# Kernel tuning notes

Measured on AMD Instinct MI355X. Metric: run time of the kernel, lower is better.

The kernel has to match this reference:

```python
import jax, jax.numpy as jnp
import numpy as np

D_MODEL = 256
N_HEADS = 8
D_K = D_MODEL // N_HEADS


def setup_inputs() -> dict:
    key = jax.random.key(0)
    ks = jax.random.split(key, 9)
    s = 1.0 / np.sqrt(D_MODEL)
    x = jax.random.normal(ks[0], (2, 4096, D_MODEL), dtype=jnp.float32)
    Wq = jax.random.uniform(ks[1], (D_MODEL, D_MODEL), minval=-s, maxval=s)
    bq = jax.random.uniform(ks[2], (D_MODEL,), minval=-s, maxval=s)
    Wk = jax.random.uniform(ks[3], (D_MODEL, D_MODEL), minval=-s, maxval=s)
    bk = jax.random.uniform(ks[4], (D_MODEL,), minval=-s, maxval=s)
    Wv = jax.random.uniform(ks[5], (D_MODEL, D_MODEL), minval=-s, maxval=s)
    bv = jax.random.uniform(ks[6], (D_MODEL,), minval=-s, maxval=s)
    Wo = jax.random.uniform(ks[7], (D_MODEL, D_MODEL), minval=-s, maxval=s)
    bo = jax.random.uniform(ks[8], (D_MODEL,), minval=-s, maxval=s)
    return {"q": x, "Wq": Wq, "bq": bq, "Wk": Wk, "bk": bk,
            "Wv": Wv, "bv": bv, "Wo": Wo, "bo": bo}


def reference(q, Wq, bq, Wk, bk, Wv, bv, Wo, bo):
    B, L, _ = q.shape
    # nn.Linear: y = x @ W.T + b ; weights stored as [out, in]
    Q = (jnp.einsum('bld,ed->ble', q, Wq) + bq).reshape(B, L, N_HEADS, D_K).transpose(0, 2, 1, 3)
    K = (jnp.einsum('bld,ed->ble', q, Wk) + bk).reshape(B, L, N_HEADS, D_K).transpose(0, 2, 1, 3)
    V = (jnp.einsum('bld,ed->ble', q, Wv) + bv).reshape(B, L, N_HEADS, D_K).transpose(0, 2, 1, 3)
    scores = jnp.einsum('bhqd,bhkd->bhqk', Q, K) / jnp.sqrt(jnp.float32(D_K))
    attn = jax.nn.softmax(scores, axis=-1)  # dropout p=0 (eval): identity
    out = jnp.einsum('bhqk,bhkd->bhqd', attn, V)
    out = out.transpose(0, 2, 1, 3).reshape(B, L, D_MODEL)
    return jnp.einsum('bld,ed->ble', out, Wo) + bo
```

## Files before the change

kernel.cpp:

```cpp
#include <hip/hip_runtime.h>

#define D_MODEL 256
#define NH 8
#define DK 32
#define SEQ 4096
#define BATCH 2
#define M_ROWS (BATCH * SEQ)
#define QSCALE 0.17677669529663687f

typedef __attribute__((ext_vector_type(8))) short bf16x8;
typedef __attribute__((ext_vector_type(4))) short s16x4;
typedef __attribute__((ext_vector_type(4))) float f32x4;
typedef __attribute__((ext_vector_type(16))) float f32x16;

static __device__ __forceinline__ short f2bf(float f) {
    unsigned u = __float_as_uint(f);
    u += 0x7fff + ((u >> 16) & 1);
    return (short)(u >> 16);
}

__global__ void cvt_kernel(const float* __restrict__ src, short* __restrict__ dst, int n4) {
    int i = blockIdx.x * blockDim.x + threadIdx.x;
    if (i >= n4) return;
    float4 v = reinterpret_cast<const float4*>(src)[i];
    s16x4 o;
    o.x = f2bf(v.x); o.y = f2bf(v.y); o.z = f2bf(v.z); o.w = f2bf(v.w);
    reinterpret_cast<s16x4*>(dst)[i] = o;
}

__global__ void cvtw_kernel(const float* __restrict__ W0, const float* __restrict__ W1,
                            const float* __restrict__ W2, const float* __restrict__ W3,
                            short* __restrict__ D0, short* __restrict__ D1,
                            short* __restrict__ D2, short* __restrict__ D3) {
    const int seg = blockIdx.x >> 6;
    const int i = (blockIdx.x & 63) * blockDim.x + threadIdx.x;
    const float* s = seg == 0 ? W0 : seg == 1 ? W1 : seg == 2 ? W2 : W3;
    short* d = seg == 0 ? D0 : seg == 1 ? D1 : seg == 2 ? D2 : D3;
    float4 v = reinterpret_cast<const float4*>(s)[i];
    s16x4 o;
    o.x = f2bf(v.x); o.y = f2bf(v.y); o.z = f2bf(v.z); o.w = f2bf(v.w);
    reinterpret_cast<s16x4*>(d)[i] = o;
}

__global__ __launch_bounds__(256) void qkv_gemm(
    const short* __restrict__ A,
    const short* __restrict__ Wqb, const short* __restrict__ Wkb, const short* __restrict__ Wvb,
    const float* __restrict__ bq, const float* __restrict__ bk, const float* __restrict__ bv,
    short* __restrict__ Qb, short* __restrict__ Kblk, short* __restrict__ Vblk)
{
    const int ct = blockIdx.x;
    const int rt = blockIdx.y;
    const int tid = threadIdx.x;
    const int w = tid >> 6, l = tid & 63, l15 = l & 15, g = l >> 4;
    const int mat = ct >> 2;
    const int colbase = (ct & 3) * 64;
    const short* W = mat == 0 ? Wqb : mat == 1 ? Wkb : Wvb;
    const float* bias = mat == 0 ? bq : mat == 1 ? bk : bv;

    const int arow = rt * 64 + w * 16 + l15;
    f32x4 acc[4] = {};
#pragma unroll
    for (int ks = 0; ks < 8; ++ks) {
        bf16x8 af = *reinterpret_cast<const bf16x8*>(&A[(size_t)arow * 256 + ks * 32 + 8 * g]);
#pragma unroll
        for (int c = 0; c < 4; ++c) {
            const int col = colbase + 16 * c + l15;
            bf16x8 wf = *reinterpret_cast<const bf16x8*>(&W[(size_t)col * 256 + ks * 32 + 8 * g]);
            acc[c] = __builtin_amdgcn_mfma_f32_16x16x32_bf16(af, wf, acc[c], 0, 0, 0);
        }
    }

#pragma unroll
    for (int c = 0; c < 4; ++c) {
        const int col = colbase + 16 * c + l15;
        const float bv_ = bias[col];
#pragma unroll
        for (int r = 0; r < 4; ++r) {
            const int m = rt * 64 + w * 16 + 4 * g + r;
            const float v = acc[c][r] + bv_;
            const int head = col >> 5, d = col & 31;
            const int bb = m >> 12, seq = m & 4095;
            const size_t bhbase = (size_t)(bb * NH + head) * (SEQ * DK);
            if (mat == 0) {
                Qb[bhbase + (size_t)seq * 32 + d] = f2bf(v * QSCALE);
            } else if (mat == 1) {
                const int t = seq >> 6, s = (seq >> 5) & 1, lk = seq & 31;
                const int hh = (d >> 4) & 1, gk = (d >> 3) & 1, jk = d & 7;
                Kblk[bhbase + t * 2048 + (s * 2 + hh) * 512 + (gk * 32 + lk) * 8 + jk] = f2bf(v);
            } else {
                const int t = seq >> 6, w6 = seq & 63;
                const int c2 = w6 >> 4, gv = (w6 >> 2) & 1, jv = ((w6 >> 3) & 1) * 4 + (w6 & 3);
                Vblk[bhbase + t * 2048 + c2 * 512 + (gv * 32 + d) * 8 + jv] = f2bf(v);
            }
        }
    }
}

__global__ __launch_bounds__(128, 4) void attn_kernel(
    const short* __restrict__ Qb, const short* __restrict__ Kblk,
    const short* __restrict__ Vblk, short* __restrict__ AOb)
{
    __shared__ float accL[64][17];

    const int bid = ((int)blockIdx.x & 7) * 256 + ((int)blockIdx.x >> 3);
    const int qt = bid & 127;
    const int bh = bid >> 7;
    const int b = bh >> 3, h = bh & 7;
    const int w = threadIdx.x >> 6;
    const int l = threadIdx.x & 63;
    const int l31 = l & 31, g1 = l >> 5;

    const short* Qh = Qb + (size_t)bh * (SEQ * DK);
    const int q0 = qt * 32;
    const bf16x8 qf0 = *(const bf16x8*)&Qh[(size_t)(q0 + l31) * 32 + g1 * 8];
    const bf16x8 qf1 = *(const bf16x8*)&Qh[(size_t)(q0 + l31) * 32 + 16 + g1 * 8];

    const char* Kt = (const char*)Kblk + (size_t)bh * 262144 + (size_t)w * 131072 + l * 16;
    const char* Vt = (const char*)Vblk + (size_t)bh * 262144 + (size_t)w * 131072 + l * 16;

    f32x16 acc;
#pragma unroll
    for (int r = 0; r < 16; ++r) acc[r] = 0.f;
    float ls0 = 0.f, ls1 = 0.f, ls2 = 0.f, ls3 = 0.f;

    auto loadt = [&](bf16x8& K0, bf16x8& K1, bf16x8& K2, bf16x8& K3,
                     bf16x8& V0, bf16x8& V1, bf16x8& V2, bf16x8& V3, int tl) {
        const char* kp = Kt + (size_t)tl * 4096;
        const char* vp = Vt + (size_t)tl * 4096;
        K0 = *(const bf16x8*)(kp);        K1 = *(const bf16x8*)(kp + 1024);
        K2 = *(const bf16x8*)(kp + 2048); K3 = *(const bf16x8*)(kp + 3072);
        V0 = *(const bf16x8*)(vp);        V1 = *(const bf16x8*)(vp + 1024);
        V2 = *(const bf16x8*)(vp + 2048); V3 = *(const bf16x8*)(vp + 3072);
    };

    auto compute = [&](const bf16x8& K0, const bf16x8& K1, const bf16x8& K2, const bf16x8& K3,
                       const bf16x8& V0, const bf16x8& V1, const bf16x8& V2, const bf16x8& V3) {
        unsigned pk[2][8];
#pragma unroll
        for (int s = 0; s < 2; ++s) {
            f32x16 z;
#pragma unroll
            for (int r = 0; r < 16; ++r) z[r] = 0.f;
            z = __builtin_amdgcn_mfma_f32_32x32x16_bf16(s ? K2 : K0, qf0, z, 0, 0, 0);
            z = __builtin_amdgcn_mfma_f32_32x32x16_bf16(s ? K3 : K1, qf1, z, 0, 0, 0);
            float e[16];
#pragma unroll
            for (int r = 0; r < 16; ++r) e[r] = __expf(z[r]);
#pragma unroll
            for (int r = 0; r < 16; r += 4) {
                ls0 += e[r]; ls1 += e[r + 1]; ls2 += e[r + 2]; ls3 += e[r + 3];
            }
#pragma unroll
            for (int i = 0; i < 8; ++i)
                asm("v_cvt_pk_bf16_f32 %0, %1, %2" : "=v"(pk[s][i]) : "v"(e[2 * i]), "v"(e[2 * i + 1]));
        }
#pragma unroll
        for (int c = 0; c < 4; ++c) {
            union { unsigned u[4]; bf16x8 bv; } pa;
#pragma unroll
            for (int i = 0; i < 4; ++i) pa.u[i] = pk[c >> 1][4 * (c & 1) + i];
            const bf16x8& vf = (c == 0) ? V0 : (c == 1) ? V1 : (c == 2) ? V2 : V3;
            acc = __builtin_amdgcn_mfma_f32_32x32x16_bf16(pa.bv, vf, acc, 0, 0, 0);
        }
    };

    bf16x8 kA0, kA1, kA2, kA3, vA0, vA1, vA2, vA3;
    bf16x8 kB0, kB1, kB2, kB3, vB0, vB1, vB2, vB3;
    loadt(kA0, kA1, kA2, kA3, vA0, vA1, vA2, vA3, 0);
    for (int i = 0; i < 16; ++i) {
        loadt(kB0, kB1, kB2, kB3, vB0, vB1, vB2, vB3, 2 * i + 1);
        compute(kA0, kA1, kA2, kA3, vA0, vA1, vA2, vA3);
        if (i < 15) loadt(kA0, kA1, kA2, kA3, vA0, vA1, vA2, vA3, 2 * i + 2);
        compute(kB0, kB1, kB2, kB3, vB0, vB1, vB2, vB3);
    }

    float ls = (ls0 + ls1) + (ls2 + ls3);
    ls += __shfl_xor(ls, 32);

    if (w == 1) {
#pragma unroll
        for (int r = 0; r < 16; ++r) accL[l][r] = acc[r];
        accL[l][16] = ls;
    }
    __syncthreads();
    if (w == 0) {
#pragma unroll
        for (int r = 0; r < 16; ++r) acc[r] += accL[l][r];
        ls += accL[l][16];
        const float inv = 1.0f / ls;
#pragma unroll
        for (int r = 0; r < 16; ++r) {
            const int ql = (r & 3) + 8 * (r >> 2) + 4 * g1;
            const float invq = __shfl(inv, ql);
            AOb[((size_t)b * SEQ + q0 + ql) * D_MODEL + h * DK + l31] = f2bf(acc[r] * invq);
        }
    }
}

__global__ __launch_bounds__(256) void out_gemm(
    const short* __restrict__ AOb, const short* __restrict__ Wob,
    const float* __restrict__ bo, float* __restrict__ out)
{
    const int ct = blockIdx.x, rt = blockIdx.y;
    const int tid = threadIdx.x;
    const int w = tid >> 6, l = tid & 63, l15 = l & 15, g = l >> 4;
    const int arow = rt * 64 + w * 16 + l15;

    f32x4 acc[4] = {};
#pragma unroll
    for (int ks = 0; ks < 8; ++ks) {
        bf16x8 af = *(const bf16x8*)&AOb[(size_t)arow * 256 + ks * 32 + 8 * g];
#pragma unroll
        for (int c = 0; c < 4; ++c) {
            const int col = ct * 64 + 16 * c + l15;
            bf16x8 wf = *(const bf16x8*)&Wob[(size_t)col * 256 + ks * 32 + 8 * g];
            acc[c] = __builtin_amdgcn_mfma_f32_16x16x32_bf16(af, wf, acc[c], 0, 0, 0);
        }
    }
#pragma unroll
    for (int c = 0; c < 4; ++c) {
        const int col = ct * 64 + 16 * c + l15;
        const float bv_ = bo[col];
#pragma unroll
        for (int r = 0; r < 4; ++r) {
            const int m = rt * 64 + w * 16 + 4 * g + r;
            out[(size_t)m * 256 + col] = acc[c][r] + bv_;
        }
    }
}

extern "C" void kernel_launch(void* const* d_in, const int* in_sizes, int n_in,
                              void* d_out, int out_size, void* d_ws, size_t ws_size,
                              hipStream_t stream) {
    const float* x  = (const float*)d_in[0];
    const float* Wq = (const float*)d_in[1];
    const float* bq = (const float*)d_in[2];
    const float* Wk = (const float*)d_in[3];
    const float* bk = (const float*)d_in[4];
    const float* Wv = (const float*)d_in[5];
    const float* bv = (const float*)d_in[6];
    const float* Wo = (const float*)d_in[7];
    const float* bo = (const float*)d_in[8];
    float* out = (float*)d_out;

    char* ws = (char*)d_ws;
    const size_t MB = 1 << 20, KB = 1 << 10;
    short* xb   = (short*)(ws);
    short* Wqb  = (short*)(ws + 4 * MB);
    short* Wkb  = (short*)(ws + 4 * MB + 128 * KB);
    short* Wvb  = (short*)(ws + 4 * MB + 256 * KB);
    short* Wob  = (short*)(ws + 4 * MB + 384 * KB);
    short* Qb   = (short*)(ws + 4 * MB + 512 * KB);
    short* Kblk = (short*)(ws + 8 * MB + 512 * KB);
    short* Vblk = (short*)(ws + 12 * MB + 512 * KB);
    short* AOb  = (short*)(ws + 16 * MB + 512 * KB);

    cvt_kernel<<<2048, 256, 0, stream>>>(x, xb, (M_ROWS * D_MODEL) / 4);
    cvtw_kernel<<<256, 256, 0, stream>>>(Wq, Wk, Wv, Wo, Wqb, Wkb, Wvb, Wob);

    dim3 gq(12, 128);
    qkv_gemm<<<gq, 256, 0, stream>>>(xb, Wqb, Wkb, Wvb, bq, bk, bv, Qb, Kblk, Vblk);

    attn_kernel<<<2048, 128, 0, stream>>>(Qb, Kblk, Vblk, AOb);

    dim3 go(4, 128);
    out_gemm<<<go, 256, 0, stream>>>(AOb, Wob, bo, out);
}
```

Measured before the change: 112.9 us.

## Split attention KV range across four waves and fuse conversion kernels

The attention block grows from two to four waves, and each wave handles a quarter of the key/value sequence. Three waves write partial accumulators and row sums to shared memory, and wave 0 reduces them. The input and weight bf16 conversion kernels are merged into one launch to save a kernel launch. Other small changes: the zero accumulator is hoisted, the P-fragment packing goes through a union, and the QK MFMA order is swapped. The extra waves should hide more latency per block, at the cost of a larger shared reduction and a higher register-occupancy target.

```diff
diff --git a/kernel.cpp b/kernel.cpp
--- a/kernel.cpp
+++ b/kernel.cpp
@@ -19,23 +19,23 @@
     return (short)(u >> 16);
 }
 
-__global__ void cvt_kernel(const float* __restrict__ src, short* __restrict__ dst, int n4) {
-    int i = blockIdx.x * blockDim.x + threadIdx.x;
-    if (i >= n4) return;
-    float4 v = reinterpret_cast<const float4*>(src)[i];
-    s16x4 o;
-    o.x = f2bf(v.x); o.y = f2bf(v.y); o.z = f2bf(v.z); o.w = f2bf(v.w);
-    reinterpret_cast<s16x4*>(dst)[i] = o;
-}
-
-__global__ void cvtw_kernel(const float* __restrict__ W0, const float* __restrict__ W1,
-                            const float* __restrict__ W2, const float* __restrict__ W3,
-                            short* __restrict__ D0, short* __restrict__ D1,
-                            short* __restrict__ D2, short* __restrict__ D3) {
-    const int seg = blockIdx.x >> 6;
-    const int i = (blockIdx.x & 63) * blockDim.x + threadIdx.x;
-    const float* s = seg == 0 ? W0 : seg == 1 ? W1 : seg == 2 ? W2 : W3;
-    short* d = seg == 0 ? D0 : seg == 1 ? D1 : seg == 2 ? D2 : D3;
+__global__ void cvt_all(const float* __restrict__ x, short* __restrict__ xb,
+                        const float* __restrict__ W0, const float* __restrict__ W1,
+                        const float* __restrict__ W2, const float* __restrict__ W3,
+                        short* __restrict__ D0, short* __restrict__ D1,
+                        short* __restrict__ D2, short* __restrict__ D3) {
+    const int blk = blockIdx.x;
+    const float* s;
+    short* d;
+    int i;
+    if (blk < 2048) {
+        s = x; d = xb; i = blk * blockDim.x + threadIdx.x;
+    } else {
+        const int seg = (blk - 2048) >> 6;
+        i = ((blk - 2048) & 63) * blockDim.x + threadIdx.x;
+        s = seg == 0 ? W0 : seg == 1 ? W1 : seg == 2 ? W2 : W3;
+        d = seg == 0 ? D0 : seg == 1 ? D1 : seg == 2 ? D2 : D3;
+    }
     float4 v = reinterpret_cast<const float4*>(s)[i];
     s16x4 o;
     o.x = f2bf(v.x); o.y = f2bf(v.y); o.z = f2bf(v.z); o.w = f2bf(v.w);
@@ -96,11 +96,11 @@
     }
 }
 
-__global__ __launch_bounds__(128, 4) void attn_kernel(
+__global__ __launch_bounds__(256, 8) void attn_kernel(
     const short* __restrict__ Qb, const short* __restrict__ Kblk,
     const short* __restrict__ Vblk, short* __restrict__ AOb)
 {
-    __shared__ float accL[64][17];
+    __shared__ float accL[3][64][17];
 
     const int bid = ((int)blockIdx.x & 7) * 256 + ((int)blockIdx.x >> 3);
     const int qt = bid & 127;
@@ -115,12 +115,15 @@
     const bf16x8 qf0 = *(const bf16x8*)&Qh[(size_t)(q0 + l31) * 32 + g1 * 8];
     const bf16x8 qf1 = *(const bf16x8*)&Qh[(size_t)(q0 + l31) * 32 + 16 + g1 * 8];
 
-    const char* Kt = (const char*)Kblk + (size_t)bh * 262144 + (size_t)w * 131072 + l * 16;
-    const char* Vt = (const char*)Vblk + (size_t)bh * 262144 + (size_t)w * 131072 + l * 16;
+    const char* Kt = (const char*)Kblk + (size_t)bh * 262144 + (size_t)w * 65536 + l * 16;
+    const char* Vt = (const char*)Vblk + (size_t)bh * 262144 + (size_t)w * 65536 + l * 16;
 
     f32x16 acc;
 #pragma unroll
     for (int r = 0; r < 16; ++r) acc[r] = 0.f;
+    f32x16 Z0;
+#pragma unroll
+    for (int r = 0; r < 16; ++r) Z0[r] = 0.f;
     float ls0 = 0.f, ls1 = 0.f, ls2 = 0.f, ls3 = 0.f;
 
     auto loadt = [&](bf16x8& K0, bf16x8& K1, bf16x8& K2, bf16x8& K3,
@@ -135,14 +138,11 @@
 
     auto compute = [&](const bf16x8& K0, const bf16x8& K1, const bf16x8& K2, const bf16x8& K3,
                        const bf16x8& V0, const bf16x8& V1, const bf16x8& V2, const bf16x8& V3) {
-        unsigned pk[2][8];
+        union { unsigned u[16]; bf16x8 v[4]; } P;
 #pragma unroll
         for (int s = 0; s < 2; ++s) {
-            f32x16 z;
-#pragma unroll
-            for (int r = 0; r < 16; ++r) z[r] = 0.f;
+            f32x16 z = __builtin_amdgcn_mfma_f32_32x32x16_bf16(s ? K3 : K1, qf1, Z0, 0, 0, 0);
             z = __builtin_amdgcn_mfma_f32_32x32x16_bf16(s ? K2 : K0, qf0, z, 0, 0, 0);
-            z = __builtin_amdgcn_mfma_f32_32x32x16_bf16(s ? K3 : K1, qf1, z, 0, 0, 0);
             float e[16];
 #pragma unroll
             for (int r = 0; r < 16; ++r) e[r] = __expf(z[r]);
@@ -152,41 +152,41 @@
             }
 #pragma unroll
             for (int i = 0; i < 8; ++i)
-                asm("v_cvt_pk_bf16_f32 %0, %1, %2" : "=v"(pk[s][i]) : "v"(e[2 * i]), "v"(e[2 * i + 1]));
+                asm("v_cvt_pk_bf16_f32 %0, %1, %2" : "=v"(P.u[s * 8 + i]) : "v"(e[2 * i]), "v"(e[2 * i + 1]));
         }
 #pragma unroll
         for (int c = 0; c < 4; ++c) {
-            union { unsigned u[4]; bf16x8 bv; } pa;
-#pragma unroll
-            for (int i = 0; i < 4; ++i) pa.u[i] = pk[c >> 1][4 * (c & 1) + i];
             const bf16x8& vf = (c == 0) ? V0 : (c == 1) ? V1 : (c == 2) ? V2 : V3;
-            acc = __builtin_amdgcn_mfma_f32_32x32x16_bf16(pa.bv, vf, acc, 0, 0, 0);
+            acc = __builtin_amdgcn_mfma_f32_32x32x16_bf16(P.v[c], vf, acc, 0, 0, 0);
         }
     };
 
     bf16x8 kA0, kA1, kA2, kA3, vA0, vA1, vA2, vA3;
     bf16x8 kB0, kB1, kB2, kB3, vB0, vB1, vB2, vB3;
     loadt(kA0, kA1, kA2, kA3, vA0, vA1, vA2, vA3, 0);
-    for (int i = 0; i < 16; ++i) {
+    for (int i = 0; i < 8; ++i) {
         loadt(kB0, kB1, kB2, kB3, vB0, vB1, vB2, vB3, 2 * i + 1);
         compute(kA0, kA1, kA2, kA3, vA0, vA1, vA2, vA3);
-        if (i < 15) loadt(kA0, kA1, kA2, kA3, vA0, vA1, vA2, vA3, 2 * i + 2);
+        if (i < 7) loadt(kA0, kA1, kA2, kA3, vA0, vA1, vA2, vA3, 2 * i + 2);
         compute(kB0, kB1, kB2, kB3, vB0, vB1, vB2, vB3);
     }
 
     float ls = (ls0 + ls1) + (ls2 + ls3);
     ls += __shfl_xor(ls, 32);
 
-    if (w == 1) {
-#pragma unroll
-        for (int r = 0; r < 16; ++r) accL[l][r] = acc[r];
-        accL[l][16] = ls;
+    if (w > 0) {
+#pragma unroll
+        for (int r = 0; r < 16; ++r) accL[w - 1][l][r] = acc[r];
+        accL[w - 1][l][16] = ls;
     }
     __syncthreads();
     if (w == 0) {
 #pragma unroll
-        for (int r = 0; r < 16; ++r) acc[r] += accL[l][r];
-        ls += accL[l][16];
+        for (int wv = 0; wv < 3; ++wv) {
+#pragma unroll
+            for (int r = 0; r < 16; ++r) acc[r] += accL[wv][l][r];
+            ls += accL[wv][l][16];
+        }
         const float inv = 1.0f / ls;
 #pragma unroll
         for (int r = 0; r < 16; ++r) {
@@ -255,13 +255,12 @@
     short* Vblk = (short*)(ws + 12 * MB + 512 * KB);
     short* AOb  = (short*)(ws + 16 * MB + 512 * KB);
 
-    cvt_kernel<<<2048, 256, 0, stream>>>(x, xb, (M_ROWS * D_MODEL) / 4);
-    cvtw_kernel<<<256, 256, 0, stream>>>(Wq, Wk, Wv, Wo, Wqb, Wkb, Wvb, Wob);
+    cvt_all<<<2304, 256, 0, stream>>>(x, xb, Wq, Wk, Wv, Wo, Wqb, Wkb, Wvb, Wob);
 
     dim3 gq(12, 128);
     qkv_gemm<<<gq, 256, 0, stream>>>(xb, Wqb, Wkb, Wvb, bq, bk, bv, Qb, Kblk, Vblk);
 
-    attn_kernel<<<2048, 128, 0, stream>>>(Qb, Kblk, Vblk, AOb);
+    attn_kernel<<<2048, 256, 0, stream>>>(Qb, Kblk, Vblk, AOb);
 
     dim3 go(4, 128);
     out_gemm<<<go, 256, 0, stream>>>(AOb, Wob, bo, out);
```

Result: slower. 440.4 us (+290.2%).
